# Kernel tuning notes

Hardware: AMD Instinct MI355X
Metric: run time of the kernel (lower is better)

Reference implementation:

```python
import jax, jax.numpy as jnp
import numpy as np

B, S, D, H = 2, 2048, 2048, 16
Dh = D // H


def _rotate_interleaved(t):
    # t: (..., Dh); pairs (x0,x1) -> (-x1, x0), interleaved
    t2 = t.reshape(t.shape[:-1] + (Dh // 2, 2))
    rot = jnp.stack([-t2[..., 1], t2[..., 0]], axis=-1)
    return rot.reshape(t.shape)


def _apply_rope(t, cos, sin):
    # t: (B,H,S,Dh); cos/sin: (S,Dh) broadcast over batch and heads
    return t * cos[None, None, :, :] + _rotate_interleaved(t) * sin[None, None, :, :]


def setup_inputs() -> dict:
    key = jax.random.key(0)
    ks = jax.random.split(key, 4)
    x = jax.random.normal(ks[0], (B, S, D), dtype=jnp.float32)
    wq = jax.random.normal(ks[1], (D, D), dtype=jnp.float32) * (D ** -0.5)
    wk = jax.random.normal(ks[2], (D, D), dtype=jnp.float32) * (D ** -0.5)
    wv = jax.random.normal(ks[3], (D, D), dtype=jnp.float32) * (D ** -0.5)
    # Real RoPE cos/sin tables: theta_i = 10000^{-2i/Dh}, interleaved layout
    inv_freq = 1.0 / (10000.0 ** (np.arange(0, Dh, 2, dtype=np.float32) / Dh))
    angles = np.arange(S, dtype=np.float32)[:, None] * inv_freq[None, :]  # (S, Dh/2)
    angles = np.repeat(angles, 2, axis=-1)  # (S, Dh) interleaved
    rope_cos = jnp.asarray(np.cos(angles))
    rope_sin = jnp.asarray(np.sin(angles))
    return {"x": x, "wq": wq, "wk": wk, "wv": wv,
            "rope_cos": rope_cos, "rope_sin": rope_sin}


def reference(x, wq, wk, wv, rope_cos, rope_sin):
    b, s, d = x.shape
    # QKV projections (torch Linear: y = x @ W^T), split into heads -> (B,H,S,Dh)
    def proj(w):
        return (x @ w.T).reshape(b, s, H, Dh).transpose(0, 2, 1, 3)
    q, k, v = proj(wq), proj(wk), proj(wv)
    cos, sin = rope_cos[:s], rope_sin[:s]
    q = _apply_rope(q, cos, sin)
    k = _apply_rope(k, cos, sin)
    # causal SDPA
    scores = jnp.einsum('bhqd,bhkd->bhqk', q, k) / jnp.sqrt(jnp.float32(Dh))
    causal = jnp.tril(jnp.ones((s, s), dtype=bool))
    scores = jnp.where(causal[None, None], scores, jnp.float32(-1e30))
    attn = jax.nn.softmax(scores, axis=-1)
    out = jnp.einsum('bhqk,bhkd->bhqd', attn, v)  # (B,H,S,Dh)
    # extra trailing softmax over head dim (as in source)
    out = jax.nn.softmax(out.astype(jnp.float32), axis=-1)
    return out.transpose(0, 2, 1, 3).reshape(b, s, -1)
```

## Files before the change

kernel.cpp:

```cpp
#include <hip/hip_runtime.h>

#define Bc 2
#define Sc 2048
#define Dc 2048
#define Hc 16
#define DHc 128

typedef _Float16 f16;
typedef __attribute__((ext_vector_type(4))) _Float16 v4h;
typedef __attribute__((ext_vector_type(8))) _Float16 v8h;
typedef __attribute__((ext_vector_type(4))) float v4f;
typedef __attribute__((ext_vector_type(16))) float v16f;
typedef __attribute__((ext_vector_type(4))) float f32x4;

__global__ void cvt_kernel(const float* __restrict__ x, const float* __restrict__ wq,
                           const float* __restrict__ wk, const float* __restrict__ wv,
                           f16* __restrict__ xh, f16* __restrict__ wqh,
                           f16* __restrict__ wkh, f16* __restrict__ wvh)
{
    int bid = blockIdx.x;
    const float* src; f16* dst; int idx;
    if (bid < 8192)       { src = x;  dst = xh;  idx = bid; }
    else if (bid < 12288) { src = wq; dst = wqh; idx = bid - 8192; }
    else if (bid < 16384) { src = wk; dst = wkh; idx = bid - 12288; }
    else                  { src = wv; dst = wvh; idx = bid - 16384; }
    int i = idx * 256 + threadIdx.x;
    f32x4 v = ((const f32x4*)src)[i];
    v4h hv; hv[0]=(f16)v[0]; hv[1]=(f16)v[1]; hv[2]=(f16)v[2]; hv[3]=(f16)v[3];
    ((v4h*)dst)[i] = hv;
}

__launch_bounds__(256)
__global__ void proj_f16_kernel(const f16* __restrict__ xh, const f16* __restrict__ wqh,
                                const f16* __restrict__ wkh, const f16* __restrict__ wvh,
                                const float* __restrict__ cs, const float* __restrict__ sn,
                                f16* __restrict__ qh, f16* __restrict__ kh,
                                f16* __restrict__ vt)
{
    const int z = blockIdx.z;
    const f16* wh = (z == 0) ? wqh : ((z == 1) ? wkh : wvh);
    const int m0 = blockIdx.x * 128, n0 = blockIdx.y * 128;
    const int tid = threadIdx.x, lane = tid & 63, wid = tid >> 6;
    const int wm = wid >> 1, wn = wid & 1;
    const int l15 = lane & 15, quad = lane >> 4;
    const int lrow = lane >> 3, lcol = lane & 7;

    __shared__ __align__(16) f16 smem[128 * 136];
    f16 (*As)[64] = (f16(*)[64])smem;
    f16 (*Bs)[64] = (f16(*)[64])(smem + 8192);

    v4f acc[4][4];
    #pragma unroll
    for (int i = 0; i < 4; ++i)
        #pragma unroll
        for (int j = 0; j < 4; ++j)
            acc[i][j] = (v4f){0.f, 0.f, 0.f, 0.f};

    for (int k0 = 0; k0 < Dc; k0 += 64) {
        __syncthreads();
        #pragma unroll
        for (int i = 0; i < 4; ++i) {
            int g = wid * 4 + i;
            const f16* ga = xh + (size_t)(m0 + g * 8 + lrow) * Dc + k0 + lcol * 8;
            __builtin_amdgcn_global_load_lds(
                (const __attribute__((address_space(1))) void*)ga,
                (__attribute__((address_space(3))) void*)(smem + g * 512), 16, 0, 0);
            const f16* gb = wh + (size_t)(n0 + g * 8 + lrow) * Dc + k0 + lcol * 8;
            __builtin_amdgcn_global_load_lds(
                (const __attribute__((address_space(1))) void*)gb,
                (__attribute__((address_space(3))) void*)(smem + 8192 + g * 512), 16, 0, 0);
        }
        __syncthreads();
        #pragma unroll
        for (int kk = 0; kk < 2; ++kk) {
            v8h af[4], bf[4];
            #pragma unroll
            for (int mi = 0; mi < 4; ++mi)
                af[mi] = *(const v8h*)&As[wm * 64 + mi * 16 + l15][kk * 32 + quad * 8];
            #pragma unroll
            for (int ni = 0; ni < 4; ++ni)
                bf[ni] = *(const v8h*)&Bs[wn * 64 + ni * 16 + l15][kk * 32 + quad * 8];
            #pragma unroll
            for (int mi = 0; mi < 4; ++mi)
                #pragma unroll
                for (int ni = 0; ni < 4; ++ni)
                    acc[mi][ni] = __builtin_amdgcn_mfma_f32_16x16x32_f16(
                        af[mi], bf[ni], acc[mi][ni], 0, 0, 0);
        }
    }
    __syncthreads();

    f16 (*Ep)[136] = (f16(*)[136])smem;
    #pragma unroll
    for (int mi = 0; mi < 4; ++mi)
        #pragma unroll
        for (int ni = 0; ni < 4; ++ni)
            #pragma unroll
            for (int r = 0; r < 4; ++r) {
                int ml = wm * 64 + mi * 16 + quad * 4 + r;
                int nl = wn * 64 + ni * 16 + l15;
                f16 val = (f16)acc[mi][ni][r];
                if (z == 2) Ep[nl][ml] = val;
                else        Ep[ml][nl] = val;
            }
    __syncthreads();

    const int b = m0 >> 11, s0 = m0 & 2047, h = n0 >> 7;
    if (z < 2) {
        f16* outp = (z == 0) ? qh : kh;
        const float scl = (z == 0) ? 0.08838834764831845f : 1.0f;
        #pragma unroll
        for (int it = 0; it < 8; ++it) {
            int ch = tid + it * 256, row = ch >> 4, c = ch & 15;
            v8h val = *(const v8h*)&Ep[row][c * 8];
            int s = s0 + row;
            const float* cp = cs + (size_t)s * DHc + c * 8;
            const float* sp = sn + (size_t)s * DHc + c * 8;
            f32x4 ca = *(const f32x4*)cp, cb = *(const f32x4*)(cp + 4);
            f32x4 sa = *(const f32x4*)sp, sb = *(const f32x4*)(sp + 4);
            float v[8];
            #pragma unroll
            for (int j = 0; j < 8; ++j) v[j] = (float)val[j];
            v8h rv;
            rv[0] = (f16)((v[0]*ca[0] - v[1]*sa[0]) * scl);
            rv[1] = (f16)((v[1]*ca[1] + v[0]*sa[1]) * scl);
            rv[2] = (f16)((v[2]*ca[2] - v[3]*sa[2]) * scl);
            rv[3] = (f16)((v[3]*ca[3] + v[2]*sa[3]) * scl);
            rv[4] = (f16)((v[4]*cb[0] - v[5]*sb[0]) * scl);
            rv[5] = (f16)((v[5]*cb[1] + v[4]*sb[1]) * scl);
            rv[6] = (f16)((v[6]*cb[2] - v[7]*sb[2]) * scl);
            rv[7] = (f16)((v[7]*cb[3] + v[6]*sb[3]) * scl);
            *(v8h*)(outp + ((size_t)((b * Hc + h) * Sc) + s0 + row) * DHc + c * 8) = rv;
        }
    } else {
        #pragma unroll
        for (int it = 0; it < 8; ++it) {
            int ch = tid + it * 256, row = ch >> 4, c = ch & 15;
            *(v8h*)(vt + ((size_t)((b * Hc + h) * DHc) + row) * Sc + s0 + c * 8) =
                *(const v8h*)&Ep[row][c * 8];
        }
    }
}

__launch_bounds__(256)
__global__ void proj_kernel(const float* __restrict__ x, const float* __restrict__ wq,
                            const float* __restrict__ wk, const float* __restrict__ wv,
                            f16* __restrict__ qh, f16* __restrict__ kh, f16* __restrict__ vt)
{
    const int z = blockIdx.z;
    const float* w = (z == 0) ? wq : ((z == 1) ? wk : wv);
    const int m0 = blockIdx.x * 128, n0 = blockIdx.y * 128;
    const int tid = threadIdx.x, lane = tid & 63, wid = tid >> 6;
    const int wm = wid >> 1, wn = wid & 1;
    const int l15 = lane & 15, quad = lane >> 4;

    __shared__ __align__(16) f16 smem[2 * 128 * 72];
    f16 (*As)[72] = (f16(*)[72])smem;
    f16 (*Bs)[72] = (f16(*)[72])(smem + 128 * 72);

    v4f acc[4][4];
    for (int i = 0; i < 4; ++i)
        for (int j = 0; j < 4; ++j)
            acc[i][j] = (v4f){0.f, 0.f, 0.f, 0.f};

    for (int k0 = 0; k0 < Dc; k0 += 64) {
        __syncthreads();
        for (int it = 0; it < 4; ++it) {
            int chunk = tid + it * 256;
            int r = chunk >> 3, cc = chunk & 7;
            const f32x4* pa = (const f32x4*)(x + (size_t)(m0 + r) * Dc + k0 + cc * 8);
            f32x4 a0 = pa[0], a1 = pa[1];
            v8h ha;
            ha[0]=(f16)a0[0]; ha[1]=(f16)a0[1]; ha[2]=(f16)a0[2]; ha[3]=(f16)a0[3];
            ha[4]=(f16)a1[0]; ha[5]=(f16)a1[1]; ha[6]=(f16)a1[2]; ha[7]=(f16)a1[3];
            *(v8h*)&As[r][cc * 8] = ha;
            const f32x4* pb = (const f32x4*)(w + (size_t)(n0 + r) * Dc + k0 + cc * 8);
            f32x4 b0 = pb[0], b1 = pb[1];
            v8h hb;
            hb[0]=(f16)b0[0]; hb[1]=(f16)b0[1]; hb[2]=(f16)b0[2]; hb[3]=(f16)b0[3];
            hb[4]=(f16)b1[0]; hb[5]=(f16)b1[1]; hb[6]=(f16)b1[2]; hb[7]=(f16)b1[3];
            *(v8h*)&Bs[r][cc * 8] = hb;
        }
        __syncthreads();
        for (int kk = 0; kk < 2; ++kk) {
            v8h af[4], bf[4];
            for (int mi = 0; mi < 4; ++mi)
                af[mi] = *(const v8h*)&As[wm * 64 + mi * 16 + l15][kk * 32 + quad * 8];
            for (int ni = 0; ni < 4; ++ni)
                bf[ni] = *(const v8h*)&Bs[wn * 64 + ni * 16 + l15][kk * 32 + quad * 8];
            for (int mi = 0; mi < 4; ++mi)
                for (int ni = 0; ni < 4; ++ni)
                    acc[mi][ni] = __builtin_amdgcn_mfma_f32_16x16x32_f16(
                        af[mi], bf[ni], acc[mi][ni], 0, 0, 0);
        }
    }
    __syncthreads();
    f16 (*Ep)[136] = (f16(*)[136])smem;
    for (int mi = 0; mi < 4; ++mi)
        for (int ni = 0; ni < 4; ++ni)
            for (int r = 0; r < 4; ++r) {
                int ml = wm * 64 + mi * 16 + quad * 4 + r;
                int nl = wn * 64 + ni * 16 + l15;
                f16 val = (f16)acc[mi][ni][r];
                if (z == 2) Ep[nl][ml] = val;
                else        Ep[ml][nl] = val;
            }
    __syncthreads();
    const int b = m0 >> 11, s0 = m0 & 2047, h = n0 >> 7;
    if (z < 2) {
        f16* outp = (z == 0) ? qh : kh;
        for (int it = 0; it < 8; ++it) {
            int ch = tid + it * 256, row = ch >> 4, c = ch & 15;
            *(v8h*)(outp + ((size_t)((b * Hc + h) * Sc) + s0 + row) * DHc + c * 8) =
                *(const v8h*)&Ep[row][c * 8];
        }
    } else {
        for (int it = 0; it < 8; ++it) {
            int ch = tid + it * 256, row = ch >> 4, c = ch & 15;
            *(v8h*)(vt + ((size_t)((b * Hc + h) * DHc) + row) * Sc + s0 + c * 8) =
                *(const v8h*)&Ep[row][c * 8];
        }
    }
}

__global__ void rope_kernel(f16* __restrict__ qh, f16* __restrict__ kh,
                            const float* __restrict__ cs, const float* __restrict__ sn)
{
    int i  = blockIdx.x * 256 + threadIdx.x;
    int d2 = i & 63;
    int s  = (i >> 6) & (Sc - 1);
    int bh = i >> 17;
    f16* t = blockIdx.y ? kh : qh;
    float scale = blockIdx.y ? 1.0f : 0.08838834764831845f;
    float c  = cs[s * DHc + 2 * d2];
    float sv = sn[s * DHc + 2 * d2];
    f16* p = t + ((size_t)bh * Sc + s) * DHc + 2 * d2;
    float t0 = (float)p[0], t1 = (float)p[1];
    p[0] = (f16)((t0 * c - t1 * sv) * scale);
    p[1] = (f16)((t1 * c + t0 * sv) * scale);
}

__launch_bounds__(256, 2)
__global__ void attn_kernel(const f16* __restrict__ qh, const f16* __restrict__ kh,
                            const f16* __restrict__ vt, float* __restrict__ out)
{
    const int L = blockIdx.x;
    const int slot = L >> 3;
    const int bh = (L & 7) * 4 + (slot >> 3);
    const int p  = slot & 7;
    const int b = bh >> 4, h = bh & 15;
    const int tid = threadIdx.x, lane = tid & 63, w = tid >> 6;
    const int l31 = lane & 31, half = lane >> 5;
    const int sw = l31 & 7;

    __shared__ __align__(16) f16 smem[32768];
    f16* ksm = smem;
    f16* vsm = smem + 16384;

    const size_t bhoff = (size_t)bh * Sc * DHc;

    const f16* ksrc[4]; const f16* vsrc[4];
    f16* kdst[4]; f16* vdst[4];
    #pragma unroll
    for (int j = 0; j < 4; ++j) {
        int slot0 = j * 256 + w * 64;
        {   int r = (slot0 >> 4) + (lane >> 4);
            int c = (lane & 15) ^ (r & 7);
            ksrc[j] = kh + bhoff + (size_t)r * DHc + c * 8;
            kdst[j] = ksm + slot0 * 8; }
        {   int r = (slot0 >> 3) + (lane >> 3);
            int c = (lane & 7) ^ (r & 7);
            vsrc[j] = vt + bhoff + (size_t)r * Sc + c * 8;
            vdst[j] = vsm + slot0 * 8; }
    }

#define STAGE(kt_, buf_) do {                                                   \
        int _ko = (kt_) * 64 * DHc;                                             \
        int _vo = (kt_) * 64;                                                   \
        int _lb = (buf_) * 8192;                                                \
        _Pragma("unroll")                                                       \
        for (int j = 0; j < 4; ++j) {                                           \
            __builtin_amdgcn_global_load_lds(                                   \
                (const __attribute__((address_space(1))) void*)(ksrc[j] + _ko), \
                (__attribute__((address_space(3))) void*)(kdst[j] + _lb), 16, 0, 0); \
            __builtin_amdgcn_global_load_lds(                                   \
                (const __attribute__((address_space(1))) void*)(vsrc[j] + _vo), \
                (__attribute__((address_space(3))) void*)(vdst[j] + _lb), 16, 0, 0); \
        } } while (0)

    const int qtA = 15 - p;
    const int nktA = 2 * qtA + 2;

    int ibuf = 0;
    STAGE(0, 0);

    #pragma unroll 1
    for (int ph = 0; ph < 2; ++ph) {
        const int qt  = ph ? p : qtA;
        const int nkt = 2 * qt + 2;
        const int q0  = qt * 128 + w * 32;
        const int qg  = q0 + l31;

        v8h qf[8];
        const f16* qrow = qh + bhoff + (size_t)qg * DHc;
        #pragma unroll
        for (int s = 0; s < 8; ++s)
            qf[s] = *(const v8h*)(qrow + s * 16 + half * 8);

        float l_run = 0.f;
        v16f o[4];
        #pragma unroll
        for (int i = 0; i < 4; ++i)
            #pragma unroll
            for (int r = 0; r < 16; ++r) o[i][r] = 0.f;

        #pragma unroll 1
        for (int kt = 0; kt < nkt; ++kt, ++ibuf) {
            __syncthreads();
            const int buf = ibuf & 1;
            const int ni = ibuf + 1;
            if (ni < 34) {
                int tn = (ni < nktA) ? ni : ni - nktA;
                STAGE(tn, ni & 1);
            }
            if (q0 + 31 < kt * 64) continue;

            const f16* kbuf = ksm + buf * 8192;
            const f16* vbuf = vsm + buf * 8192;
            const bool do1 = (kt * 64 + 32 <= q0 + 31);

            v16f st0, st1;
            #pragma unroll
            for (int r = 0; r < 16; ++r) { st0[r] = 0.f; st1[r] = 0.f; }
            #pragma unroll
            for (int s = 0; s < 8; ++s) {
                int c = ((s * 2 + half) ^ sw) * 8;
                v8h kf0 = *(const v8h*)(kbuf + l31 * 128 + c);
                st0 = __builtin_amdgcn_mfma_f32_32x32x16_f16(kf0, qf[s], st0, 0, 0, 0);
                if (do1) {
                    v8h kf1 = *(const v8h*)(kbuf + (32 + l31) * 128 + c);
                    st1 = __builtin_amdgcn_mfma_f32_32x32x16_f16(kf1, qf[s], st1, 0, 0, 0);
                }
            }

            float sum = 0.f;
            #pragma unroll
            for (int r = 0; r < 16; ++r) {
                int key = kt * 64 + (r & 3) + 8 * (r >> 2) + 4 * half;
                float sv = (key > qg) ? -1e30f : st0[r];
                float pe = __expf(sv);
                st0[r] = pe; sum += pe;
            }
            if (do1) {
                #pragma unroll
                for (int r = 0; r < 16; ++r) {
                    int key = kt * 64 + 32 + (r & 3) + 8 * (r >> 2) + 4 * half;
                    float sv = (key > qg) ? -1e30f : st1[r];
                    float pe = __expf(sv);
                    st1[r] = pe; sum += pe;
                }
            }
            sum += __shfl_xor(sum, 32);
            l_run += sum;

            #pragma unroll
            for (int s2 = 0; s2 < 4; ++s2) {
                v4h bfr;
                bfr[0]=(f16)st0[4*s2]; bfr[1]=(f16)st0[4*s2+1];
                bfr[2]=(f16)st0[4*s2+2]; bfr[3]=(f16)st0[4*s2+3];
                int c = ((s2 ^ sw) * 8) + half * 4;
                #pragma unroll
                for (int dt = 0; dt < 4; ++dt) {
                    v4h vf = *(const v4h*)(vbuf + (dt * 32 + l31) * 64 + c);
                    o[dt] = __builtin_amdgcn_mfma_f32_32x32x8f16(vf, bfr, o[dt], 0, 0, 0);
                }
            }
            if (do1) {
                #pragma unroll
                for (int s2 = 0; s2 < 4; ++s2) {
                    v4h bfr;
                    bfr[0]=(f16)st1[4*s2]; bfr[1]=(f16)st1[4*s2+1];
                    bfr[2]=(f16)st1[4*s2+2]; bfr[3]=(f16)st1[4*s2+3];
                    int c = (((4 + s2) ^ sw) * 8) + half * 4;
                    #pragma unroll
                    for (int dt = 0; dt < 4; ++dt) {
                        v4h vf = *(const v4h*)(vbuf + (dt * 32 + l31) * 64 + c);
                        o[dt] = __builtin_amdgcn_mfma_f32_32x32x8f16(vf, bfr, o[dt], 0, 0, 0);
                    }
                }
            }
        }

        float inv = 1.f / l_run;
        float mxd = -1e30f;
        #pragma unroll
        for (int dt = 0; dt < 4; ++dt)
            #pragma unroll
            for (int r = 0; r < 16; ++r) {
                o[dt][r] *= inv;
                mxd = fmaxf(mxd, o[dt][r]);
            }
        mxd = fmaxf(mxd, __shfl_xor(mxd, 32));
        float sd = 0.f;
        #pragma unroll
        for (int dt = 0; dt < 4; ++dt)
            #pragma unroll
            for (int r = 0; r < 16; ++r) {
                float t = __expf(o[dt][r] - mxd);
                o[dt][r] = t;
                sd += t;
            }
        sd += __shfl_xor(sd, 32);
        float rinv = 1.f / sd;

        float* orow = out + (size_t)(b * Sc + qg) * Dc + h * DHc;
        #pragma unroll
        for (int dt = 0; dt < 4; ++dt)
            #pragma unroll
            for (int g = 0; g < 4; ++g) {
                f32x4 vv;
                vv[0] = o[dt][4*g+0] * rinv;
                vv[1] = o[dt][4*g+1] * rinv;
                vv[2] = o[dt][4*g+2] * rinv;
                vv[3] = o[dt][4*g+3] * rinv;
                *(f32x4*)(orow + dt * 32 + g * 8 + half * 4) = vv;
            }
    }
#undef STAGE
}

extern "C" void kernel_launch(void* const* d_in, const int* in_sizes, int n_in,
                              void* d_out, int out_size, void* d_ws, size_t ws_size,
                              hipStream_t stream)
{
    const float* x  = (const float*)d_in[0];
    const float* wq = (const float*)d_in[1];
    const float* wk = (const float*)d_in[2];
    const float* wv = (const float*)d_in[3];
    const float* cs = (const float*)d_in[4];
    const float* sn = (const float*)d_in[5];
    float* out = (float*)d_out;

    const size_t tsz = (size_t)Bc * Hc * Sc * DHc;
    f16* qh = (f16*)d_ws;
    f16* kh = qh + tsz;
    f16* vt = kh + tsz;

    if (ws_size >= 11 * tsz) {
        f16* xh  = vt + tsz;
        f16* wqh = xh + tsz;
        f16* wkh = wqh + tsz / 2;
        f16* wvh = wkh + tsz / 2;
        cvt_kernel<<<20480, 256, 0, stream>>>(x, wq, wk, wv, xh, wqh, wkh, wvh);
        proj_f16_kernel<<<dim3(32, 16, 3), 256, 0, stream>>>(xh, wqh, wkh, wvh,
                                                             cs, sn, qh, kh, vt);
    } else {
        proj_kernel<<<dim3(32, 16, 3), 256, 0, stream>>>(x, wq, wk, wv, qh, kh, vt);
        rope_kernel<<<dim3(16384, 2), 256, 0, stream>>>(qh, kh, cs, sn);
    }
    attn_kernel<<<256, 256, 0, stream>>>(qh, kh, vt, out);
}
```

Before: 355.9 us.

## Rewrite QKV projection GEMM with 128x256 tiles, double-buffered LDS, swizzle

Replaces the 128x128 single-buffered projection GEMM with a 512-thread kernel that computes 128x256 tiles over the concatenated Wq/Wk/Wv weights. It double-buffers LDS with register-level fragment prefetch and XOR-swizzles LDS columns to avoid bank conflicts. It also remaps block IDs for L2 locality and raises MFMA priority. The aim is to hide global-load latency and raise MFMA utilisation, at the cost of more LDS and registers per block and an epilogue that relies on the three weight buffers being contiguous.

```diff
diff --git a/kernel.cpp b/kernel.cpp
--- a/kernel.cpp
+++ b/kernel.cpp
@@ -30,24 +30,84 @@
     ((v4h*)dst)[i] = hv;
 }
 
-__launch_bounds__(256)
-__global__ void proj_f16_kernel(const f16* __restrict__ xh, const f16* __restrict__ wqh,
-                                const f16* __restrict__ wkh, const f16* __restrict__ wvh,
-                                const float* __restrict__ cs, const float* __restrict__ sn,
-                                f16* __restrict__ qh, f16* __restrict__ kh,
-                                f16* __restrict__ vt)
+__launch_bounds__(512, 2)
+__global__ void proj256_kernel(const f16* __restrict__ xh, const f16* __restrict__ wall,
+                               const float* __restrict__ cs, const float* __restrict__ sn,
+                               f16* __restrict__ qh, f16* __restrict__ kh,
+                               f16* __restrict__ vt)
 {
-    const int z = blockIdx.z;
-    const f16* wh = (z == 0) ? wqh : ((z == 1) ? wkh : wvh);
-    const int m0 = blockIdx.x * 128, n0 = blockIdx.y * 128;
-    const int tid = threadIdx.x, lane = tid & 63, wid = tid >> 6;
-    const int wm = wid >> 1, wn = wid & 1;
+    const int bid = blockIdx.x;
+    const int swz = (bid & 7) * 96 + (bid >> 3);
+    const int mt = swz & 31, nt = swz >> 5;
+    const int m0 = mt * 128, n0 = nt * 256;
+
+    const int tid = threadIdx.x;
+    const int wid = tid >> 6, lane = tid & 63;
+    const int wr = wid >> 2, wc = wid & 3;
     const int l15 = lane & 15, quad = lane >> 4;
-    const int lrow = lane >> 3, lcol = lane & 7;
-
-    __shared__ __align__(16) f16 smem[128 * 136];
-    f16 (*As)[64] = (f16(*)[64])smem;
-    f16 (*Bs)[64] = (f16(*)[64])(smem + 8192);
+    const int x7 = l15 & 7;
+
+    __shared__ __align__(16) f16 lds[49152];
+
+    const f16* aS[2]; const f16* bS[4];
+    #pragma unroll
+    for (int j = 0; j < 2; ++j) {
+        int c = tid + j * 512;
+        int r = c >> 3, s = c & 7;
+        aS[j] = xh + (size_t)(m0 + r) * Dc + ((s ^ (r & 7)) * 8);
+    }
+    #pragma unroll
+    for (int j = 0; j < 4; ++j) {
+        int c = tid + j * 512;
+        int r = c >> 3, s = c & 7;
+        bS[j] = wall + (size_t)(n0 + r) * Dc + ((s ^ (r & 7)) * 8);
+    }
+
+#define STAGE(kt_, buf_) do {                                                   \
+        const int _ko = (kt_) * 64;                                             \
+        f16* _b = lds + (buf_) * 24576;                                         \
+        _Pragma("unroll")                                                       \
+        for (int j = 0; j < 2; ++j)                                             \
+            __builtin_amdgcn_global_load_lds(                                   \
+                (const __attribute__((address_space(1))) void*)(aS[j] + _ko),   \
+                (__attribute__((address_space(3))) void*)(_b + j * 4096 + wid * 512), \
+                16, 0, 0);                                                      \
+        _Pragma("unroll")                                                       \
+        for (int j = 0; j < 4; ++j)                                             \
+            __builtin_amdgcn_global_load_lds(                                   \
+                (const __attribute__((address_space(1))) void*)(bS[j] + _ko),   \
+                (__attribute__((address_space(3))) void*)(_b + 8192 + j * 4096 + wid * 512), \
+                16, 0, 0);                                                      \
+    } while (0)
+
+#define RDFRAG(af_, bf_, buf_) do {                                             \
+        const f16* _Ab = lds + (buf_) * 24576;                                  \
+        const f16* _Bb = _Ab + 8192;                                            \
+        _Pragma("unroll")                                                       \
+        for (int kk = 0; kk < 2; ++kk) {                                        \
+            _Pragma("unroll")                                                   \
+            for (int mi = 0; mi < 4; ++mi)                                      \
+                af_[kk][mi] = *(const v8h*)(_Ab + (wr * 64 + mi * 16 + l15) * 64 \
+                                            + (((kk * 4 + quad) ^ x7) * 8));    \
+            _Pragma("unroll")                                                   \
+            for (int ni = 0; ni < 4; ++ni)                                      \
+                bf_[kk][ni] = *(const v8h*)(_Bb + (wc * 64 + ni * 16 + l15) * 64 \
+                                            + (((kk * 4 + quad) ^ x7) * 8));    \
+        }                                                                       \
+    } while (0)
+
+#define MM(af_, bf_) do {                                                       \
+        __builtin_amdgcn_s_setprio(1);                                          \
+        _Pragma("unroll")                                                       \
+        for (int kk = 0; kk < 2; ++kk)                                          \
+            _Pragma("unroll")                                                   \
+            for (int mi = 0; mi < 4; ++mi)                                      \
+                _Pragma("unroll")                                               \
+                for (int ni = 0; ni < 4; ++ni)                                  \
+                    acc[mi][ni] = __builtin_amdgcn_mfma_f32_16x16x32_f16(       \
+                        af_[kk][mi], bf_[kk][ni], acc[mi][ni], 0, 0, 0);        \
+        __builtin_amdgcn_s_setprio(0);                                          \
+    } while (0)
 
     v4f acc[4][4];
     #pragma unroll
@@ -56,66 +116,55 @@
         for (int j = 0; j < 4; ++j)
             acc[i][j] = (v4f){0.f, 0.f, 0.f, 0.f};
 
-    for (int k0 = 0; k0 < Dc; k0 += 64) {
+    v8h afA[2][4], bfA[2][4], afB[2][4], bfB[2][4];
+
+    STAGE(0, 0);
+    STAGE(1, 1);
+    __syncthreads();
+    RDFRAG(afA, bfA, 0);
+    __syncthreads();
+
+    #pragma unroll 1
+    for (int t = 0; t < 32; t += 2) {
+        if (t + 2 < 32) STAGE(t + 2, 0);
+        RDFRAG(afB, bfB, 1);
+        MM(afA, bfA);
         __syncthreads();
-        #pragma unroll
-        for (int i = 0; i < 4; ++i) {
-            int g = wid * 4 + i;
-            const f16* ga = xh + (size_t)(m0 + g * 8 + lrow) * Dc + k0 + lcol * 8;
-            __builtin_amdgcn_global_load_lds(
-                (const __attribute__((address_space(1))) void*)ga,
-                (__attribute__((address_space(3))) void*)(smem + g * 512), 16, 0, 0);
-            const f16* gb = wh + (size_t)(n0 + g * 8 + lrow) * Dc + k0 + lcol * 8;
-            __builtin_amdgcn_global_load_lds(
-                (const __attribute__((address_space(1))) void*)gb,
-                (__attribute__((address_space(3))) void*)(smem + 8192 + g * 512), 16, 0, 0);
-        }
+        if (t + 3 < 32) STAGE(t + 3, 1);
+        if (t + 2 < 32) RDFRAG(afA, bfA, 0);
+        MM(afB, bfB);
         __syncthreads();
-        #pragma unroll
-        for (int kk = 0; kk < 2; ++kk) {
-            v8h af[4], bf[4];
-            #pragma unroll
-            for (int mi = 0; mi < 4; ++mi)
-                af[mi] = *(const v8h*)&As[wm * 64 + mi * 16 + l15][kk * 32 + quad * 8];
+    }
+
+#undef STAGE
+#undef RDFRAG
+#undef MM
+
+    const int z = n0 >> 11;
+    const int bb = m0 >> 11, s0 = m0 & 2047;
+
+    if (z < 2) {
+        f16 (*Ep)[264] = (f16(*)[264])lds;
+        #pragma unroll
+        for (int mi = 0; mi < 4; ++mi)
             #pragma unroll
             for (int ni = 0; ni < 4; ++ni)
-                bf[ni] = *(const v8h*)&Bs[wn * 64 + ni * 16 + l15][kk * 32 + quad * 8];
-            #pragma unroll
-            for (int mi = 0; mi < 4; ++mi)
                 #pragma unroll
-                for (int ni = 0; ni < 4; ++ni)
-                    acc[mi][ni] = __builtin_amdgcn_mfma_f32_16x16x32_f16(
-                        af[mi], bf[ni], acc[mi][ni], 0, 0, 0);
-        }
-    }
-    __syncthreads();
-
-    f16 (*Ep)[136] = (f16(*)[136])smem;
-    #pragma unroll
-    for (int mi = 0; mi < 4; ++mi)
-        #pragma unroll
-        for (int ni = 0; ni < 4; ++ni)
-            #pragma unroll
-            for (int r = 0; r < 4; ++r) {
-                int ml = wm * 64 + mi * 16 + quad * 4 + r;
-                int nl = wn * 64 + ni * 16 + l15;
-                f16 val = (f16)acc[mi][ni][r];
-                if (z == 2) Ep[nl][ml] = val;
-                else        Ep[ml][nl] = val;
-            }
-    __syncthreads();
-
-    const int b = m0 >> 11, s0 = m0 & 2047, h = n0 >> 7;
-    if (z < 2) {
+                for (int r = 0; r < 4; ++r)
+                    Ep[wr * 64 + mi * 16 + quad * 4 + r][wc * 64 + ni * 16 + l15] =
+                        (f16)acc[mi][ni][r];
+        __syncthreads();
         f16* outp = (z == 0) ? qh : kh;
         const float scl = (z == 0) ? 0.08838834764831845f : 1.0f;
         #pragma unroll
         for (int it = 0; it < 8; ++it) {
-            int ch = tid + it * 256, row = ch >> 4, c = ch & 15;
+            int ch = tid + it * 512, row = ch >> 5, c = ch & 31;
             v8h val = *(const v8h*)&Ep[row][c * 8];
             int s = s0 + row;
-            const float* cp = cs + (size_t)s * DHc + c * 8;
-            const float* sp = sn + (size_t)s * DHc + c * 8;
+            int nn = (n0 & 2047) + c * 8;
+            int h = nn >> 7, d0 = nn & 127;
+            const float* cp = cs + (size_t)s * DHc + d0;
+            const float* sp = sn + (size_t)s * DHc + d0;
             f32x4 ca = *(const f32x4*)cp, cb = *(const f32x4*)(cp + 4);
             f32x4 sa = *(const f32x4*)sp, sb = *(const f32x4*)(sp + 4);
             float v[8];
@@ -130,14 +179,27 @@
             rv[5] = (f16)((v[5]*cb[1] + v[4]*sb[1]) * scl);
             rv[6] = (f16)((v[6]*cb[2] - v[7]*sb[2]) * scl);
             rv[7] = (f16)((v[7]*cb[3] + v[6]*sb[3]) * scl);
-            *(v8h*)(outp + ((size_t)((b * Hc + h) * Sc) + s0 + row) * DHc + c * 8) = rv;
+            *(v8h*)(outp + ((size_t)(bb * Hc + h) * Sc + s) * DHc + d0) = rv;
         }
     } else {
+        f16 (*Ep)[136] = (f16(*)[136])lds;
+        #pragma unroll
+        for (int mi = 0; mi < 4; ++mi)
+            #pragma unroll
+            for (int ni = 0; ni < 4; ++ni)
+                #pragma unroll
+                for (int r = 0; r < 4; ++r)
+                    Ep[wc * 64 + ni * 16 + l15][wr * 64 + mi * 16 + quad * 4 + r] =
+                        (f16)acc[mi][ni][r];
+        __syncthreads();
         #pragma unroll
         for (int it = 0; it < 8; ++it) {
-            int ch = tid + it * 256, row = ch >> 4, c = ch & 15;
-            *(v8h*)(vt + ((size_t)((b * Hc + h) * DHc) + row) * Sc + s0 + c * 8) =
-                *(const v8h*)&Ep[row][c * 8];
+            int ch = tid + it * 512, n = ch >> 4, cm = ch & 15;
+            int nn = (n0 & 2047) + n;
+            int h = nn >> 7, d = nn & 127;
+            int s = s0 + cm * 8;
+            *(v8h*)(vt + ((size_t)(bb * Hc + h) * DHc + d) * Sc + s) =
+                *(const v8h*)&Ep[n][cm * 8];
         }
     }
 }
@@ -452,8 +514,7 @@
         f16* wkh = wqh + tsz / 2;
         f16* wvh = wkh + tsz / 2;
         cvt_kernel<<<20480, 256, 0, stream>>>(x, wq, wk, wv, xh, wqh, wkh, wvh);
-        proj_f16_kernel<<<dim3(32, 16, 3), 256, 0, stream>>>(xh, wqh, wkh, wvh,
-                                                             cs, sn, qh, kh, vt);
+        proj256_kernel<<<768, 512, 0, stream>>>(xh, wqh, cs, sn, qh, kh, vt);
     } else {
         proj_kernel<<<dim3(32, 16, 3), 256, 0, stream>>>(x, wq, wk, wv, qh, kh, vt);
         rope_kernel<<<dim3(16384, 2), 256, 0, stream>>>(qh, kh, cs, sn);
```

New measurement: 342.0 us. 1.04x faster.
